# Kernel tuning notes

Hardware: AMD Instinct MI355X
Metric: run time of the kernel (lower is better)

## Reference

```python
import jax, jax.numpy as jnp
import numpy as np

N, D_IN, D_OUT = 16384, 64, 64
AVG_DEG = 32.0
L2_EPS = 1e-12  # torch F.normalize default eps


def setup_inputs() -> dict:
    key = jax.random.key(0)
    kx, ka, kw, kb = jax.random.split(key, 4)
    X = jax.random.normal(kx, (N, D_IN), dtype=jnp.float32)
    # binary adjacency with avg degree ~AVG_DEG (module treats adj as 0/1 mask)
    adj = (jax.random.uniform(ka, (N, N)) < (AVG_DEG / N)).astype(jnp.float32)
    # nn.Linear(2*D_IN, D_OUT): store W as (2*D_IN, D_OUT) for x @ W + b
    bound = 1.0 / np.sqrt(2 * D_IN)
    W = jax.random.uniform(kw, (2 * D_IN, D_OUT), dtype=jnp.float32, minval=-bound, maxval=bound)
    b = jax.random.uniform(kb, (D_OUT,), dtype=jnp.float32, minval=-bound, maxval=bound)
    return {"X": X, "adj": adj, "W": W, "b": b}


def reference(X, adj, W, b):
    # eval-mode mean aggregation: h_neigh = (adj + I) @ X / clamp(rowsum(adj + I), 1)
    # (adj + I) @ X == adj @ X + X, avoiding materializing the NxN identity.
    deg = jnp.clip(jnp.sum(adj, axis=1, keepdims=True) + 1.0, 1.0, None)  # (N,1)
    h_neigh = (adj @ X + X) / deg                                          # (N,D)
    concat = jnp.concatenate([X, h_neigh], axis=1)                         # (N,2D)
    z = concat @ W + b                                                     # (N,O)
    out = jax.nn.relu(z)
    norm = jnp.linalg.norm(out, axis=1, keepdims=True)
    return out / jnp.maximum(norm, L2_EPS)
```

## Files before the change

### kernel.cpp

```cpp
#include <hip/hip_runtime.h>
#include <stdint.h>


#define NROWS   16384
#define DDIM    64
#define MAXNNZ  256
#define NBLOCKS 4096

typedef uint32_t u32x4 __attribute__((ext_vector_type(4)));

__device__ __forceinline__ int lane_rank(unsigned long long m) {
    return __builtin_amdgcn_mbcnt_hi((uint32_t)(m >> 32),
           __builtin_amdgcn_mbcnt_lo((uint32_t)m, 0));
}

__global__ __launch_bounds__(256, 4) void sage_fused(
    const float* __restrict__ X,
    const float* __restrict__ adj,
    const float* __restrict__ W,
    const float* __restrict__ bias,
    float* __restrict__ out)
{
    __shared__ int   slist[4][MAXNNZ];
    __shared__ float scat[4][2 * DDIM];

    const int tid  = threadIdx.x;
    const int lane = tid & 63;
    const int w    = tid >> 6;
    const int row  = blockIdx.x * 4 + w;

    const float bv = bias[lane];

    const int start = (row * 7 + (row >> 4)) & 15;
    const u32x4* rowp = reinterpret_cast<const u32x4*>(adj + (size_t)row * NROWS);

    u32x4 buf[2][4];
    {
        const int ss0 = start;
        const int ss1 = (start + 1) & 15;
#pragma unroll
        for (int q = 0; q < 4; ++q)
            buf[0][q] = __builtin_nontemporal_load(&rowp[ss0 * 256 + q * 64 + lane]);
#pragma unroll
        for (int q = 0; q < 4; ++q)
            buf[1][q] = __builtin_nontemporal_load(&rowp[ss1 * 256 + q * 64 + lane]);
    }

    int cnt = 0;

#pragma unroll 2
    for (int s = 0; s < 16; ++s) {
        const int cur = s & 1;
        const int ss  = (s + start) & 15;

        u32x4 t[4];
#pragma unroll
        for (int q = 0; q < 4; ++q) t[q] = buf[cur][q];

        if (s < 14) {
            const int ssn = (s + 2 + start) & 15;
#pragma unroll
            for (int q = 0; q < 4; ++q)
                buf[cur][q] = __builtin_nontemporal_load(&rowp[ssn * 256 + q * 64 + lane]);
        }

#pragma unroll
        for (int q = 0; q < 4; ++q) {
            const u32x4 vv = t[q];
            const int base = (ss * 256 + q * 64 + lane) * 4;
            const uint32_t w4[4] = { vv.x, vv.y, vv.z, vv.w };
#pragma unroll
            for (int j = 0; j < 4; ++j) {
                const bool nz = (w4[j] != 0);
                const unsigned long long m = __ballot(nz);
                const int p = cnt + lane_rank(m);
                if (nz && p < MAXNNZ) slist[w][p] = base + j;
                cnt += (int)__popcll(m);
            }
        }
    }
    __builtin_amdgcn_wave_barrier();

    const int nnz = cnt;
    const int cn  = (nnz < MAXNNZ) ? nnz : MAXNNZ;

    float acc = 0.0f;
    int k = 0;
    for (; k + 4 <= cn; k += 4) {
        const int j0 = slist[w][k], j1 = slist[w][k + 1];
        const int j2 = slist[w][k + 2], j3 = slist[w][k + 3];
        const float a0 = X[(size_t)j0 * DDIM + lane];
        const float a1 = X[(size_t)j1 * DDIM + lane];
        const float a2 = X[(size_t)j2 * DDIM + lane];
        const float a3 = X[(size_t)j3 * DDIM + lane];
        acc += (a0 + a1) + (a2 + a3);
    }
    for (; k < cn; ++k) acc += X[(size_t)slist[w][k] * DDIM + lane];

    const float xi = X[(size_t)row * DDIM + lane];
    const float h  = (acc + xi) / ((float)nnz + 1.0f);
    scat[w][lane]        = xi;
    scat[w][DDIM + lane] = h;
    __builtin_amdgcn_wave_barrier();

    float z0 = bv, z1 = 0.0f, z2 = 0.0f, z3 = 0.0f;
#pragma unroll 8
    for (int kk = 0; kk < 2 * DDIM; kk += 4) {
        z0 = fmaf(scat[w][kk + 0], W[(kk + 0) * DDIM + lane], z0);
        z1 = fmaf(scat[w][kk + 1], W[(kk + 1) * DDIM + lane], z1);
        z2 = fmaf(scat[w][kk + 2], W[(kk + 2) * DDIM + lane], z2);
        z3 = fmaf(scat[w][kk + 3], W[(kk + 3) * DDIM + lane], z3);
    }
    float z = (z0 + z1) + (z2 + z3);
    z = fmaxf(z, 0.0f);

    float s2 = z * z;
#pragma unroll
    for (int off = 32; off >= 1; off >>= 1) s2 += __shfl_xor(s2, off);
    const float inv = 1.0f / fmaxf(sqrtf(s2), 1e-12f);
    out[(size_t)row * DDIM + lane] = z * inv;
}

extern "C" void kernel_launch(void* const* d_in, const int* in_sizes, int n_in,
                              void* d_out, int out_size, void* d_ws, size_t ws_size,
                              hipStream_t stream) {
    const float* X   = (const float*)d_in[0];
    const float* adj = (const float*)d_in[1];
    const float* W   = (const float*)d_in[2];
    const float* b   = (const float*)d_in[3];
    float* out = (float*)d_out;
    sage_fused<<<NBLOCKS, 256, 0, stream>>>(X, adj, W, b, out);
}
```

Before: 1.291 ms.

## Stream adjacency rows via async global-to-LDS loads with four-deep pipeline

Replaces the register-double-buffered nontemporal loads of each adjacency row with direct global_load_lds transfers into a per-wave four-slot LDS ring, waiting on vmcnt before extracting each chunk. This deepens the prefetch of the dominant dense adj stream to hide more memory latency without holding buffers in registers. It also drops the staggered start offset per row and the nontemporal hint, and adds 32KB of LDS per block, which may reduce occupancy.

```diff
diff --git a/kernel.cpp b/kernel.cpp
--- a/kernel.cpp
+++ b/kernel.cpp
@@ -6,8 +6,16 @@
 #define DDIM    64
 #define MAXNNZ  256
 #define NBLOCKS 4096
+#define NCHUNK  32
 
 typedef uint32_t u32x4 __attribute__((ext_vector_type(4)));
+
+#define GL2LDS(g, l)                                                        \
+    __builtin_amdgcn_global_load_lds(                                       \
+        (const __attribute__((address_space(1))) void*)(g),                 \
+        (__attribute__((address_space(3))) void*)(l), 16, 0, 0)
+
+#define WAITVM(n) asm volatile("s_waitcnt vmcnt(" #n ")" ::: "memory")
 
 __device__ __forceinline__ int lane_rank(unsigned long long m) {
     return __builtin_amdgcn_mbcnt_hi((uint32_t)(m >> 32),
@@ -21,64 +29,62 @@
     const float* __restrict__ bias,
     float* __restrict__ out)
 {
-    __shared__ int   slist[4][MAXNNZ];
-    __shared__ float scat[4][2 * DDIM];
+    __shared__ uint32_t stage[4][4][512];
+    __shared__ int      slist[4][MAXNNZ];
+    __shared__ float    scat[4][2 * DDIM];
 
     const int tid  = threadIdx.x;
     const int lane = tid & 63;
     const int w    = tid >> 6;
     const int row  = blockIdx.x * 4 + w;
 
-    const float bv = bias[lane];
+    const float* rowp = adj + (size_t)row * NROWS;
 
-    const int start = (row * 7 + (row >> 4)) & 15;
-    const u32x4* rowp = reinterpret_cast<const u32x4*>(adj + (size_t)row * NROWS);
-
-    u32x4 buf[2][4];
-    {
-        const int ss0 = start;
-        const int ss1 = (start + 1) & 15;
 #pragma unroll
-        for (int q = 0; q < 4; ++q)
-            buf[0][q] = __builtin_nontemporal_load(&rowp[ss0 * 256 + q * 64 + lane]);
-#pragma unroll
-        for (int q = 0; q < 4; ++q)
-            buf[1][q] = __builtin_nontemporal_load(&rowp[ss1 * 256 + q * 64 + lane]);
+    for (int c = 0; c < 4; ++c) {
+        const float* g = rowp + c * 512 + lane * 4;
+        uint32_t* lp = &stage[w][c][0];
+        GL2LDS(g,       lp);
+        GL2LDS(g + 256, lp + 256);
     }
 
     int cnt = 0;
 
-#pragma unroll 2
-    for (int s = 0; s < 16; ++s) {
-        const int cur = s & 1;
-        const int ss  = (s + start) & 15;
+#define EXTRACT(C)                                                           \
+    {                                                                        \
+        __builtin_amdgcn_sched_barrier(0);                                   \
+        const u32x4* sp = reinterpret_cast<const u32x4*>(&stage[w][(C) & 3][0]); \
+        _Pragma("unroll")                                                    \
+        for (int k = 0; k < 2; ++k) {                                        \
+            const u32x4 vv = sp[k * 64 + lane];                              \
+            const int base = (C) * 512 + k * 256 + lane * 4;                 \
+            const uint32_t w4[4] = { vv.x, vv.y, vv.z, vv.w };               \
+            _Pragma("unroll")                                                \
+            for (int j = 0; j < 4; ++j) {                                    \
+                const bool nz = (w4[j] != 0);                                \
+                const unsigned long long m = __ballot(nz);                   \
+                const int p = cnt + lane_rank(m);                            \
+                if (nz && p < MAXNNZ) slist[w][p] = base + j;                \
+                cnt += (int)__popcll(m);                                     \
+            }                                                                \
+        }                                                                    \
+    }
 
-        u32x4 t[4];
-#pragma unroll
-        for (int q = 0; q < 4; ++q) t[q] = buf[cur][q];
+    for (int c = 0; c < NCHUNK - 4; ++c) {
+        WAITVM(6);
+        EXTRACT(c);
+        const int cn4 = c + 4;
+        const float* g = rowp + cn4 * 512 + lane * 4;
+        uint32_t* lp = &stage[w][cn4 & 3][0];
+        GL2LDS(g,       lp);
+        GL2LDS(g + 256, lp + 256);
+    }
+    WAITVM(6); EXTRACT(NCHUNK - 4);
+    WAITVM(4); EXTRACT(NCHUNK - 3);
+    WAITVM(2); EXTRACT(NCHUNK - 2);
+    WAITVM(0); EXTRACT(NCHUNK - 1);
+#undef EXTRACT
 
-        if (s < 14) {
-            const int ssn = (s + 2 + start) & 15;
-#pragma unroll
-            for (int q = 0; q < 4; ++q)
-                buf[cur][q] = __builtin_nontemporal_load(&rowp[ssn * 256 + q * 64 + lane]);
-        }
-
-#pragma unroll
-        for (int q = 0; q < 4; ++q) {
-            const u32x4 vv = t[q];
-            const int base = (ss * 256 + q * 64 + lane) * 4;
-            const uint32_t w4[4] = { vv.x, vv.y, vv.z, vv.w };
-#pragma unroll
-            for (int j = 0; j < 4; ++j) {
-                const bool nz = (w4[j] != 0);
-                const unsigned long long m = __ballot(nz);
-                const int p = cnt + lane_rank(m);
-                if (nz && p < MAXNNZ) slist[w][p] = base + j;
-                cnt += (int)__popcll(m);
-            }
-        }
-    }
     __builtin_amdgcn_wave_barrier();
 
     const int nnz = cnt;
@@ -103,6 +109,7 @@
     scat[w][DDIM + lane] = h;
     __builtin_amdgcn_wave_barrier();
 
+    const float bv = bias[lane];
     float z0 = bv, z1 = 0.0f, z2 = 0.0f, z3 = 0.0f;
 #pragma unroll 8
     for (int kk = 0; kk < 2 * DDIM; kk += 4) {
```

Result: slower. 1.344 ms (+4.2%).
